# Performance work log

Hardware: AMD Instinct MI355X
Metric: run time of the kernel (lower is better)

The kernel has to match this reference:

```python
import jax, jax.numpy as jnp
import numpy as np

N = 50000      # nodes
E = 1_600_000  # edges (avg degree 32)
H = 32         # hidden_dim
ED = 16        # edge_dim
L = 4          # num EGNN layers
F_IN = 23      # prot_in_dim
LN_EPS = 1e-5


def setup_inputs() -> dict:
    key = jax.random.key(0)
    ks = jax.random.split(key, 24)
    s = 0.1  # param init scale
    inp = {
        "node_pos": jax.random.normal(ks[0], (N, 3), jnp.float32) * 10.0,
        "node_feat": jax.random.normal(ks[1], (N, F_IN), jnp.float32),
        "edge_attr": jax.random.normal(ks[2], (E, ED), jnp.float32),
        "proj_w": jax.random.normal(ks[3], (F_IN, H), jnp.float32) * s,
        "proj_b": jnp.zeros((H,), jnp.float32),
        # phi_e: Linear(2H+ED+1 -> H), SiLU, Linear(H -> H)   [stacked over L layers]
        "pe_w1": jax.random.normal(ks[4], (L, 2 * H + ED + 1, H), jnp.float32) * s,
        "pe_b1": jnp.zeros((L, H), jnp.float32),
        "pe_w2": jax.random.normal(ks[5], (L, H, H), jnp.float32) * s,
        "pe_b2": jnp.zeros((L, H), jnp.float32),
        # phi_h: Linear(2H -> H), SiLU, Linear(H -> H)
        "ph_w1": jax.random.normal(ks[6], (L, 2 * H, H), jnp.float32) * s,
        "ph_b1": jnp.zeros((L, H), jnp.float32),
        "ph_w2": jax.random.normal(ks[7], (L, H, H), jnp.float32) * s,
        "ph_b2": jnp.zeros((L, H), jnp.float32),
        # phi_x: Linear(H -> H), SiLU, Linear(H -> 1)
        "px_w1": jax.random.normal(ks[8], (L, H, H), jnp.float32) * s,
        "px_b1": jnp.zeros((L, H), jnp.float32),
        "px_w2": jax.random.normal(ks[9], (L, H, 1), jnp.float32) * s,
        "px_b2": jnp.zeros((L, 1), jnp.float32),
        # LayerNorm per layer
        "ln_g": jnp.ones((L, H), jnp.float32),
        "ln_b": jnp.zeros((L, H), jnp.float32),
        "edge_index": jax.random.randint(ks[10], (2, E), 0, N, dtype=jnp.int32),
    }
    return inp


def _mlp2(x, w1, b1, w2, b2):
    # Linear -> SiLU -> Linear (dropout=0 / eval mode)
    return jax.nn.silu(x @ w1 + b1) @ w2 + b2


def _layernorm(x, g, b):
    mu = jnp.mean(x, axis=-1, keepdims=True)
    var = jnp.mean(jnp.square(x - mu), axis=-1, keepdims=True)
    return (x - mu) * jax.lax.rsqrt(var + LN_EPS) * g + b


def reference(node_pos, node_feat, edge_attr, proj_w, proj_b,
              pe_w1, pe_b1, pe_w2, pe_b2,
              ph_w1, ph_b1, ph_w2, ph_b2,
              px_w1, px_b1, px_w2, px_b2,
              ln_g, ln_b, edge_index):
    src = edge_index[0]
    dst = edge_index[1]
    n = node_feat.shape[0]

    h = node_feat @ proj_w + proj_b  # (N,H)
    x = node_pos                     # (N,3)

    for l in range(L):
        h_i = h[src]                 # (E,H)
        h_j = h[dst]                 # (E,H)
        x_i = x[src]                 # (E,3)
        x_j = x[dst]                 # (E,3)
        diff = x_j - x_i             # (E,3)
        dist = jnp.sqrt(jnp.sum(diff * diff, axis=-1, keepdims=True) + 1e-09)  # (E,1)

        m_in = jnp.concatenate([h_i, h_j, edge_attr, dist], axis=-1)  # (E, 2H+ED+1)
        m_ij = _mlp2(m_in, pe_w1[l], pe_b1[l], pe_w2[l], pe_b2[l])    # (E,H)

        agg = jax.ops.segment_sum(m_ij, dst, num_segments=n)          # (N,H)
        dh = _mlp2(jnp.concatenate([h, agg], axis=-1),
                   ph_w1[l], ph_b1[l], ph_w2[l], ph_b2[l])            # (N,H)
        h = _layernorm(h + dh, ln_g[l], ln_b[l])

        # coordinate update: x_j += sum_i unit(x_j - x_i) * phi_x(m_ij)
        dir_norm = jnp.linalg.norm(diff, axis=-1, keepdims=True) + 1e-09
        gate = _mlp2(m_ij, px_w1[l], px_b1[l], px_w2[l], px_b2[l])    # (E,1)
        coord_msg = (diff / dir_norm) * gate                          # (E,3)
        dx = jax.ops.segment_sum(coord_msg, dst, num_segments=n)      # (N,3)
        x = x + dx

    return h, x
```

## Files before the change

kernel.cpp:

```cpp
#include <hip/hip_runtime.h>
#include <hip/hip_fp16.h>
#include <math.h>

#define NN 50000
#define NE 1600000
#define H  32
#define ED 16
#define FIN 23
#define NL 4
#define CPAD 16
#define LW 19

union F4 { float4 v; float f[4]; };

__device__ __forceinline__ float silu_f(float v) {
    float e = __expf(-v);
    return v * __builtin_amdgcn_rcpf(1.0f + e);
}

__device__ __forceinline__ void acc4(float hid[H], float4 hv4, const float* __restrict__ w) {
    F4 u; u.v = hv4;
    #pragma unroll
    for (int jj = 0; jj < 4; ++jj) {
        float v = u.f[jj];
        #pragma unroll
        for (int k = 0; k < H; ++k) hid[k] = fmaf(v, w[jj * H + k], hid[k]);
    }
}


__global__ __launch_bounds__(256) void k_prep(
    const float* __restrict__ pe_w2, const float* __restrict__ pe_b2,
    const float* __restrict__ px_w1, const float* __restrict__ px_b1,
    float* __restrict__ w2x, float* __restrict__ cvec)
{
    int l = blockIdx.x;
    const float* w2  = pe_w2 + (size_t)l * H * H;
    const float* xw1 = px_w1 + (size_t)l * H * H;
    int tid = threadIdx.x;
    #pragma unroll
    for (int q = 0; q < 4; ++q) {
        int idx = q * 256 + tid;
        int j = idx >> 5, k = idx & 31;
        float acc = 0.0f;
        #pragma unroll
        for (int t = 0; t < H; ++t) acc = fmaf(w2[j * H + t], xw1[t * H + k], acc);
        w2x[(size_t)l * H * H + idx] = acc;
    }
    if (tid < H) {
        const float* b2 = pe_b2 + l * H;
        float acc = px_b1[l * H + tid];
        #pragma unroll
        for (int t = 0; t < H; ++t) acc = fmaf(b2[t], xw1[t * H + tid], acc);
        cvec[l * H + tid] = acc;
    }
}


__global__ __launch_bounds__(256) void k_hist(
    const int* __restrict__ edst, int* __restrict__ cnt, int* __restrict__ rank)
{
    int e = blockIdx.x * 256 + threadIdx.x;
    if (e >= NE) return;
    rank[e] = atomicAdd(&cnt[(size_t)edst[e] * CPAD], 1);
}

__global__ __launch_bounds__(1024) void k_scan(
    const int* __restrict__ cnt, int* __restrict__ rs)
{
    __shared__ int wsum[16];
    __shared__ int s_carry;
    int t = threadIdx.x;
    int lane = t & 63, wid = t >> 6;
    if (t == 0) s_carry = 0;
    __syncthreads();
    for (int base = 0; base < NN; base += 1024) {
        int i = base + t;
        int v = (i < NN) ? cnt[(size_t)i * CPAD] : 0;
        int incl = v;
        #pragma unroll
        for (int off = 1; off < 64; off <<= 1) {
            int u = __shfl_up(incl, off, 64);
            if (lane >= off) incl += u;
        }
        if (lane == 63) wsum[wid] = incl;
        __syncthreads();
        int wpre = 0;
        #pragma unroll
        for (int w = 0; w < 16; ++w) { int ws = wsum[w]; wpre += (w < wid) ? ws : 0; }
        int carry = s_carry;
        if (i < NN) rs[i] = carry + wpre + incl - v;
        __syncthreads();
        if (t == 1023) s_carry = carry + wpre + incl;
        __syncthreads();
    }
    if (t == 0) rs[NN] = s_carry;
}

__global__ __launch_bounds__(256) void k_scatter2(
    const int* __restrict__ esrc, const int* __restrict__ edst,
    const int* __restrict__ rank, const int* __restrict__ rs,
    const float* __restrict__ ea,
    float* __restrict__ ea_s, unsigned int* __restrict__ sdp)
{
    int e = blockIdx.x * 256 + threadIdx.x;
    if (e >= NE) return;
    int s = esrc[e], d = edst[e];
    int slot = rs[d] + rank[e];
    const float4* src4 = (const float4*)(ea + (size_t)e * ED);
    float4* dst4 = (float4*)(ea_s + (size_t)slot * ED);
    #pragma unroll
    for (int j = 0; j < ED / 4; ++j) dst4[j] = src4[j];
    sdp[slot] = (unsigned int)s | ((unsigned int)d << 16);
}


__global__ __launch_bounds__(256) void proj2(
    const float* __restrict__ feat, const float* __restrict__ pos,
    const float* __restrict__ W, const float* __restrict__ bias,
    const float* __restrict__ pew1,
    float* __restrict__ h, float* __restrict__ a, float* __restrict__ b,
    float4* __restrict__ xp)
{
    int n = blockIdx.x * 256 + threadIdx.x;
    if (n >= NN) return;
    float acc[H];
    #pragma unroll
    for (int k = 0; k < H; ++k) acc[k] = bias[k];
    #pragma unroll 1
    for (int j = 0; j < FIN; ++j) {
        float v = feat[n * FIN + j];
        const float* w = W + j * H;
        #pragma unroll
        for (int k = 0; k < H; ++k) acc[k] = fmaf(v, w[k], acc[k]);
    }
    float4* h4 = (float4*)(h + (size_t)n * H);
    #pragma unroll
    for (int k4 = 0; k4 < H / 4; ++k4) {
        float4 o;
        o.x = acc[4*k4+0]; o.y = acc[4*k4+1]; o.z = acc[4*k4+2]; o.w = acc[4*k4+3];
        h4[k4] = o;
    }
    float pa[H];
    #pragma unroll
    for (int k = 0; k < H; ++k) pa[k] = 0.0f;
    #pragma unroll 1
    for (int j = 0; j < H; ++j) {
        float v = acc[j];
        const float* w = pew1 + j * H;
        #pragma unroll
        for (int k = 0; k < H; ++k) pa[k] = fmaf(v, w[k], pa[k]);
    }
    float4* a4 = (float4*)(a + (size_t)n * H);
    #pragma unroll
    for (int k4 = 0; k4 < H / 4; ++k4) {
        float4 o;
        o.x = pa[4*k4+0]; o.y = pa[4*k4+1]; o.z = pa[4*k4+2]; o.w = pa[4*k4+3];
        a4[k4] = o;
    }
    #pragma unroll
    for (int k = 0; k < H; ++k) pa[k] = 0.0f;
    #pragma unroll 1
    for (int j = 0; j < H; ++j) {
        float v = acc[j];
        const float* w = pew1 + (H + j) * H;
        #pragma unroll
        for (int k = 0; k < H; ++k) pa[k] = fmaf(v, w[k], pa[k]);
    }
    float4* b4 = (float4*)(b + (size_t)n * H);
    #pragma unroll
    for (int k4 = 0; k4 < H / 4; ++k4) {
        float4 o;
        o.x = pa[4*k4+0]; o.y = pa[4*k4+1]; o.z = pa[4*k4+2]; o.w = pa[4*k4+3];
        b4[k4] = o;
    }
    float4 xo;
    xo.x = pos[3*n+0]; xo.y = pos[3*n+1]; xo.z = pos[3*n+2]; xo.w = 0.0f;
    xp[n] = xo;
}


__global__ __launch_bounds__(256) void egnn_edge5(
    const float* __restrict__ a, const float* __restrict__ b,
    const float4* __restrict__ xp,
    const float* __restrict__ ea_s, const unsigned int* __restrict__ sdp,
    const float* __restrict__ w1, const float* __restrict__ b1,
    const float* __restrict__ w2x, const float* __restrict__ cvec,
    const float* __restrict__ xw2, const float* __restrict__ xb2,
    float* __restrict__ agg, float* __restrict__ dxb)
{
    __shared__ unsigned int ldsu[256 * LW];
    __shared__ int s_start[4][66];
    __shared__ int s_dstv[4][64];
    __shared__ int s_nseg[4];

    int tid = threadIdx.x;
    int w = tid >> 6, lane = tid & 63;
    int slot = blockIdx.x * 256 + tid;

    unsigned int sd = sdp[slot];
    int s = (int)(sd & 0xffffu), d = (int)(sd >> 16);

    float hid[H];
    const float4* av = (const float4*)(a + (size_t)s * H);
    const float4* bv = (const float4*)(b + (size_t)d * H);
    #pragma unroll
    for (int k4 = 0; k4 < H / 4; ++k4) {
        F4 ua, ub; ua.v = av[k4]; ub.v = bv[k4];
        #pragma unroll
        for (int jj = 0; jj < 4; ++jj)
            hid[4*k4+jj] = b1[4*k4+jj] + ua.f[jj] + ub.f[jj];
    }

    const float4* eav = (const float4*)(ea_s + (size_t)slot * ED);
    #pragma unroll 1
    for (int j4 = 0; j4 < ED / 4; ++j4)
        acc4(hid, eav[j4], w1 + (2 * H + j4 * 4) * H);

    float4 xi = xp[s];
    float4 xj = xp[d];
    float d0 = xj.x - xi.x, d1 = xj.y - xi.y, d2 = xj.z - xi.z;
    float sq = d0*d0 + d1*d1 + d2*d2;
    float dist = __builtin_amdgcn_sqrtf(sq + 1e-9f);
    {
        const float* wl = w1 + (2 * H + ED) * H;
        #pragma unroll
        for (int k = 0; k < H; ++k) hid[k] = fmaf(dist, wl[k], hid[k]);
    }

    float sarr[H];
    float gh[H];
    #pragma unroll
    for (int k = 0; k < H; ++k) gh[k] = cvec[k];
    #pragma unroll
    for (int j = 0; j < H; ++j) {
        float v = silu_f(hid[j]);
        sarr[j] = v;
        const float* ww = w2x + j * H;
        #pragma unroll
        for (int k = 0; k < H; ++k) gh[k] = fmaf(v, ww[k], gh[k]);
    }

    float gate = xb2[0];
    #pragma unroll
    for (int j = 0; j < H; ++j) gate = fmaf(silu_f(gh[j]), xw2[j], gate);
    float scale = gate * __builtin_amdgcn_rcpf(__builtin_amdgcn_sqrtf(sq) + 1e-9f);

    unsigned int* row = &ldsu[tid * LW];
    #pragma unroll
    for (int k2 = 0; k2 < 16; ++k2) {
        __half2 hh = __floats2half2_rn(sarr[2*k2], sarr[2*k2+1]);
        row[k2] = *reinterpret_cast<unsigned int*>(&hh);
    }
    row[16] = __float_as_uint(d0 * scale);
    row[17] = __float_as_uint(d1 * scale);
    row[18] = __float_as_uint(d2 * scale);

    int dprev = __shfl_up(d, 1, 64);
    bool flag = (lane == 0) || (d != dprev);
    unsigned long long ball = __ballot(flag);
    unsigned long long mask_le = (lane == 63) ? ~0ull : ((1ull << (lane + 1)) - 1ull);
    int segid = __popcll(ball & mask_le) - 1;
    if (flag) { s_start[w][segid] = lane; s_dstv[w][segid] = d; }
    if (lane == 0) {
        int ns = __popcll(ball);
        s_start[w][ns] = 64;
        s_nseg[w] = ns;
    }
    __syncthreads();

    int nseg = s_nseg[w];
    const unsigned int* wrows = &ldsu[(w * 64) * LW];
    int sub = lane >> 5, col = lane & 31;
    int word = col >> 1, sh = (col & 1) * 16;
    #pragma unroll 1
    for (int sg = sub; sg < nseg; sg += 2) {
        int r0 = s_start[w][sg], r1 = s_start[w][sg + 1];
        float v = 0.0f;
        #pragma unroll 1
        for (int r = r0; r < r1; ++r) {
            unsigned int u = wrows[r * LW + word];
            v += __half2float(__ushort_as_half((unsigned short)(u >> sh)));
        }
        unsafeAtomicAdd(&agg[(size_t)s_dstv[w][sg] * H + col], v);
    }
    #pragma unroll 1
    for (int j = lane; j < nseg * 4; j += 64) {
        int sg = j >> 2, c = j & 3;
        if (c < 3) {
            int r0 = s_start[w][sg], r1 = s_start[w][sg + 1];
            float v = 0.0f;
            #pragma unroll 1
            for (int r = r0; r < r1; ++r) v += __uint_as_float(wrows[r * LW + 16 + c]);
            unsafeAtomicAdd(&dxb[(size_t)s_dstv[w][sg] * 4 + c], v);
        }
    }
}


__global__ __launch_bounds__(256) void egnn_node5(
    const float* __restrict__ h, const float* __restrict__ agg,
    const float4* __restrict__ xin, const float* __restrict__ dxb,
    const int* __restrict__ rs,
    const float* __restrict__ ew2, const float* __restrict__ eb2,
    const float* __restrict__ w1, const float* __restrict__ b1,
    const float* __restrict__ w2, const float* __restrict__ b2,
    const float* __restrict__ lng, const float* __restrict__ lnb,
    const float* __restrict__ nxtw1, int last,
    float* __restrict__ hout, float* __restrict__ xout,
    float* __restrict__ aout, float* __restrict__ bout)
{
    int n = blockIdx.x * 256 + threadIdx.x;
    if (n >= NN) return;
    const float4* h4 = (const float4*)(h + (size_t)n * H);
    const float4* a4 = (const float4*)(agg + (size_t)n * H);

    float degf = (float)(rs[n + 1] - rs[n]);
    float ma[H];
    #pragma unroll
    for (int k = 0; k < H; ++k) ma[k] = degf * eb2[k];
    #pragma unroll 1
    for (int j4 = 0; j4 < H / 4; ++j4)
        acc4(ma, a4[j4], ew2 + (j4 * 4) * H);

    float hv[H];
    float hid[H];
    #pragma unroll
    for (int k = 0; k < H; ++k) hid[k] = b1[k];
    #pragma unroll 1
    for (int j4 = 0; j4 < H / 4; ++j4) {
        F4 u; u.v = h4[j4];
        #pragma unroll
        for (int jj = 0; jj < 4; ++jj) hv[4*j4+jj] = u.f[jj];
        acc4(hid, u.v, w1 + (j4 * 4) * H);
    }
    #pragma unroll
    for (int j = 0; j < H; ++j) {
        float v = ma[j];
        const float* ww = w1 + (H + j) * H;
        #pragma unroll
        for (int k = 0; k < H; ++k) hid[k] = fmaf(v, ww[k], hid[k]);
    }

    float dh[H];
    #pragma unroll
    for (int k = 0; k < H; ++k) dh[k] = b2[k];
    #pragma unroll
    for (int j = 0; j < H; ++j) {
        float v = silu_f(hid[j]);
        const float* ww = w2 + j * H;
        #pragma unroll
        for (int k = 0; k < H; ++k) dh[k] = fmaf(v, ww[k], dh[k]);
    }

    float y[H];
    float mu = 0.0f;
    #pragma unroll
    for (int k = 0; k < H; ++k) { y[k] = hv[k] + dh[k]; mu += y[k]; }
    mu *= (1.0f / H);
    float var = 0.0f;
    #pragma unroll
    for (int k = 0; k < H; ++k) { float t = y[k] - mu; var += t * t; }
    var *= (1.0f / H);
    float rstd = rsqrtf(var + 1e-5f);

    float hn[H];
    #pragma unroll
    for (int k = 0; k < H; ++k) hn[k] = (y[k] - mu) * rstd * lng[k] + lnb[k];

    float4* ho4 = (float4*)(hout + (size_t)n * H);
    #pragma unroll
    for (int k4 = 0; k4 < H / 4; ++k4) {
        float4 o;
        o.x = hn[4*k4+0]; o.y = hn[4*k4+1]; o.z = hn[4*k4+2]; o.w = hn[4*k4+3];
        ho4[k4] = o;
    }

    float4 xi = xin[n];
    float nx0 = xi.x + dxb[(size_t)n * 4 + 0];
    float nx1 = xi.y + dxb[(size_t)n * 4 + 1];
    float nx2 = xi.z + dxb[(size_t)n * 4 + 2];
    if (last) {
        xout[3*n+0] = nx0; xout[3*n+1] = nx1; xout[3*n+2] = nx2;
    } else {
        float4 o; o.x = nx0; o.y = nx1; o.z = nx2; o.w = 0.0f;
        ((float4*)xout)[n] = o;
    }

    if (!last) {
        float pa[H];
        #pragma unroll
        for (int k = 0; k < H; ++k) pa[k] = 0.0f;
        #pragma unroll 1
        for (int j = 0; j < H; ++j) {
            float v = hn[j];
            const float* ww = nxtw1 + j * H;
            #pragma unroll
            for (int k = 0; k < H; ++k) pa[k] = fmaf(v, ww[k], pa[k]);
        }
        float4* ao4 = (float4*)(aout + (size_t)n * H);
        #pragma unroll
        for (int k4 = 0; k4 < H / 4; ++k4) {
            float4 o;
            o.x = pa[4*k4+0]; o.y = pa[4*k4+1]; o.z = pa[4*k4+2]; o.w = pa[4*k4+3];
            ao4[k4] = o;
        }
        #pragma unroll
        for (int k = 0; k < H; ++k) pa[k] = 0.0f;
        #pragma unroll 1
        for (int j = 0; j < H; ++j) {
            float v = hn[j];
            const float* ww = nxtw1 + (H + j) * H;
            #pragma unroll
            for (int k = 0; k < H; ++k) pa[k] = fmaf(v, ww[k], pa[k]);
        }
        float4* bo4 = (float4*)(bout + (size_t)n * H);
        #pragma unroll
        for (int k4 = 0; k4 < H / 4; ++k4) {
            float4 o;
            o.x = pa[4*k4+0]; o.y = pa[4*k4+1]; o.z = pa[4*k4+2]; o.w = pa[4*k4+3];
            bo4[k4] = o;
        }
    }
}

extern "C" void kernel_launch(void* const* d_in, const int* in_sizes, int n_in,
                              void* d_out, int out_size, void* d_ws, size_t ws_size,
                              hipStream_t stream) {
    const float* node_pos  = (const float*)d_in[0];
    const float* node_feat = (const float*)d_in[1];
    const float* edge_attr = (const float*)d_in[2];
    const float* proj_w    = (const float*)d_in[3];
    const float* proj_b    = (const float*)d_in[4];
    const float* pe_w1     = (const float*)d_in[5];
    const float* pe_b1     = (const float*)d_in[6];
    const float* pe_w2     = (const float*)d_in[7];
    const float* pe_b2     = (const float*)d_in[8];
    const float* ph_w1     = (const float*)d_in[9];
    const float* ph_b1     = (const float*)d_in[10];
    const float* ph_w2     = (const float*)d_in[11];
    const float* ph_b2     = (const float*)d_in[12];
    const float* px_w1     = (const float*)d_in[13];
    const float* px_b1     = (const float*)d_in[14];
    const float* px_w2     = (const float*)d_in[15];
    const float* px_b2     = (const float*)d_in[16];
    const float* ln_g      = (const float*)d_in[17];
    const float* ln_b      = (const float*)d_in[18];
    const int*   eidx      = (const int*)d_in[19];
    const int*   esrc      = eidx;
    const int*   edst      = eidx + NE;

    float* out_h = (float*)d_out;
    float* out_x = out_h + (size_t)NN * H;

    size_t off = 0;
    float* ea_s = (float*)d_ws;                off += (size_t)NE * ED;
    unsigned int* sdp = (unsigned int*)((float*)d_ws + off); off += NE;
    float* abuf = (float*)d_ws + off;          off += (size_t)NN * H;
    float* bbuf = (float*)d_ws + off;          off += (size_t)NN * H;
    float* h_a  = (float*)d_ws + off;          off += (size_t)NN * H;
    float* h_b  = (float*)d_ws + off;          off += (size_t)NN * H;
    float4* xp_a = (float4*)((float*)d_ws + off); off += (size_t)NN * 4;
    float4* xp_b = (float4*)((float*)d_ws + off); off += (size_t)NN * 4;
    float* agg  = (float*)d_ws + off;          off += (size_t)NN * H;
    float* dxb  = (float*)d_ws + off;          off += (size_t)NN * 4;
    float* w2x  = (float*)d_ws + off;          off += (size_t)NL * H * H;
    float* cvec = (float*)d_ws + off;          off += (size_t)NL * H;
    int*   cnt  = (int*)((float*)d_ws + off);  off += (size_t)NN * CPAD;
    int*   rs   = (int*)((float*)d_ws + off);  off += NN + 4;
    int*   rank = (int*)((float*)d_ws + off);  off += NE;

    dim3 nblk((NN + 255) / 256), eblk(NE / 256);

    hipMemsetAsync(cnt, 0, (size_t)NN * CPAD * sizeof(int), stream);
    k_hist<<<eblk, 256, 0, stream>>>(edst, cnt, rank);
    k_scan<<<1, 1024, 0, stream>>>(cnt, rs);
    k_scatter2<<<eblk, 256, 0, stream>>>(esrc, edst, rank, rs, edge_attr, ea_s, sdp);
    k_prep<<<dim3(NL), 256, 0, stream>>>(pe_w2, pe_b2, px_w1, px_b1, w2x, cvec);

    proj2<<<nblk, 256, 0, stream>>>(node_feat, node_pos, proj_w, proj_b, pe_w1,
                                    h_a, abuf, bbuf, xp_a);

    const float* hcur = h_a;
    const float4* xcur = xp_a;
    float* hbufs[2] = { h_b, h_a };
    float4* xbufs[2] = { xp_b, xp_a };

    for (int l = 0; l < NL; ++l) {
        hipMemsetAsync(agg, 0, (size_t)NN * (H + 4) * sizeof(float), stream);
        egnn_edge5<<<eblk, 256, 0, stream>>>(abuf, bbuf, xcur, ea_s, sdp,
            pe_w1 + (size_t)l * (2*H + ED + 1) * H, pe_b1 + l * H,
            w2x + (size_t)l * H * H,               cvec + l * H,
            px_w2 + (size_t)l * H,                 px_b2 + l,
            agg, dxb);
        int last = (l == NL - 1);
        float* ho = last ? out_h : hbufs[l & 1];
        float* xo = last ? out_x : (float*)xbufs[l & 1];
        const float* nxtw1 = last ? pe_w1 : (pe_w1 + (size_t)(l + 1) * (2*H + ED + 1) * H);
        egnn_node5<<<nblk, 256, 0, stream>>>(hcur, agg, xcur, dxb, rs,
            pe_w2 + (size_t)l * H * H, pe_b2 + l * H,
            ph_w1 + (size_t)l * 2 * H * H, ph_b1 + l * H,
            ph_w2 + (size_t)l * H * H,     ph_b2 + l * H,
            ln_g + l * H, ln_b + l * H,
            nxtw1, last, ho, xo, abuf, bbuf);
        hcur = ho;
        xcur = xbufs[l & 1];
    }
}
```

Baseline: 1.160 ms.

## Use packed fp16 dot products for edge MLP and restructure segment reduction

Edge attributes and the fused w2·px_w1 weight are stored as packed fp16 pairs, so the edge kernel's inner products use v_dot2 instructions, halving FMA count and edge-attribute bandwidth. The segment reduction now walks the wave ballot mask directly with shuffles instead of building LDS segment tables behind a block barrier. The per-layer memset of agg/dxb is replaced by zeroing inside the node kernel after it reads them. This trades some accuracy, since more of the pipeline runs in fp16 with round-toward-zero packing, for less ALU work and fewer launches.

```diff
diff --git a/kernel.cpp b/kernel.cpp
--- a/kernel.cpp
+++ b/kernel.cpp
@@ -8,10 +8,24 @@
 #define ED 16
 #define FIN 23
 #define NL 4
+#define W1ROWS 81
 #define CPAD 16
 #define LW 19
 
+typedef _Float16 hv2 __attribute__((ext_vector_type(2)));
+typedef __fp16   fv2 __attribute__((ext_vector_type(2)));
+union H2U { unsigned int u; hv2 h; fv2 f; };
 union F4 { float4 v; float f[4]; };
+
+__device__ __forceinline__ unsigned int pack2(float a, float b) {
+    H2U r; r.f = __builtin_amdgcn_cvt_pkrtz(a, b);
+    return r.u;
+}
+
+__device__ __forceinline__ float fdot2f(unsigned int a, unsigned int b, float c) {
+    H2U ua, ub; ua.u = a; ub.u = b;
+    return __builtin_amdgcn_fdot2(ua.h, ub.h, c, false);
+}
 
 __device__ __forceinline__ float silu_f(float v) {
     float e = __expf(-v);
@@ -30,10 +44,13 @@
 
 
 __global__ __launch_bounds__(256) void k_prep(
-    const float* __restrict__ pe_w2, const float* __restrict__ pe_b2,
+    const float* __restrict__ pe_w1, const float* __restrict__ pe_w2,
+    const float* __restrict__ pe_b2,
     const float* __restrict__ px_w1, const float* __restrict__ px_b1,
-    float* __restrict__ w2x, float* __restrict__ cvec)
-{
+    unsigned int* __restrict__ w1h, unsigned int* __restrict__ w2xh,
+    float* __restrict__ cvec)
+{
+    __shared__ float w2x[H * H];
     int l = blockIdx.x;
     const float* w2  = pe_w2 + (size_t)l * H * H;
     const float* xw1 = px_w1 + (size_t)l * H * H;
@@ -45,11 +62,23 @@
         float acc = 0.0f;
         #pragma unroll
         for (int t = 0; t < H; ++t) acc = fmaf(w2[j * H + t], xw1[t * H + k], acc);
-        w2x[(size_t)l * H * H + idx] = acc;
+        w2x[idx] = acc;
+    }
+    __syncthreads();
+    #pragma unroll
+    for (int q = 0; q < 2; ++q) {
+        int i2 = q * 256 + tid;
+        int j2 = i2 >> 5, k = i2 & 31;
+        w2xh[(size_t)l * 512 + i2] = pack2(w2x[(2*j2) * H + k], w2x[(2*j2+1) * H + k]);
+    }
+    {
+        int j2 = tid >> 5, k = tid & 31;
+        const float* w1 = pe_w1 + (size_t)l * W1ROWS * H;
+        w1h[(size_t)l * 256 + tid] = pack2(w1[(2*H + 2*j2) * H + k], w1[(2*H + 2*j2+1) * H + k]);
     }
     if (tid < H) {
+        float acc = px_b1[l * H + tid];
         const float* b2 = pe_b2 + l * H;
-        float acc = px_b1[l * H + tid];
         #pragma unroll
         for (int t = 0; t < H; ++t) acc = fmaf(b2[t], xw1[t * H + tid], acc);
         cvec[l * H + tid] = acc;
@@ -101,16 +130,20 @@
     const int* __restrict__ esrc, const int* __restrict__ edst,
     const int* __restrict__ rank, const int* __restrict__ rs,
     const float* __restrict__ ea,
-    float* __restrict__ ea_s, unsigned int* __restrict__ sdp)
+    unsigned int* __restrict__ ea_h, unsigned int* __restrict__ sdp)
 {
     int e = blockIdx.x * 256 + threadIdx.x;
     if (e >= NE) return;
     int s = esrc[e], d = edst[e];
     int slot = rs[d] + rank[e];
     const float4* src4 = (const float4*)(ea + (size_t)e * ED);
-    float4* dst4 = (float4*)(ea_s + (size_t)slot * ED);
-    #pragma unroll
-    for (int j = 0; j < ED / 4; ++j) dst4[j] = src4[j];
+    uint2* dst2 = (uint2*)(ea_h + (size_t)slot * 8);
+    #pragma unroll
+    for (int j = 0; j < ED / 4; ++j) {
+        float4 v = src4[j];
+        uint2 o; o.x = pack2(v.x, v.y); o.y = pack2(v.z, v.w);
+        dst2[j] = o;
+    }
     sdp[slot] = (unsigned int)s | ((unsigned int)d << 16);
 }
 
@@ -180,19 +213,17 @@
 }
 
 
-__global__ __launch_bounds__(256) void egnn_edge5(
+__global__ __launch_bounds__(256) void egnn_edge6(
     const float* __restrict__ a, const float* __restrict__ b,
     const float4* __restrict__ xp,
-    const float* __restrict__ ea_s, const unsigned int* __restrict__ sdp,
-    const float* __restrict__ w1, const float* __restrict__ b1,
-    const float* __restrict__ w2x, const float* __restrict__ cvec,
+    const unsigned int* __restrict__ ea_h, const unsigned int* __restrict__ sdp,
+    const unsigned int* __restrict__ w1h, const float* __restrict__ b1,
+    const float* __restrict__ w1,
+    const unsigned int* __restrict__ w2xh, const float* __restrict__ cvec,
     const float* __restrict__ xw2, const float* __restrict__ xb2,
     float* __restrict__ agg, float* __restrict__ dxb)
 {
-    __shared__ unsigned int ldsu[256 * LW];
-    __shared__ int s_start[4][66];
-    __shared__ int s_dstv[4][64];
-    __shared__ int s_nseg[4];
+    __shared__ unsigned int ldsu[256 * LW + 4];
 
     int tid = threadIdx.x;
     int w = tid >> 6, lane = tid & 63;
@@ -212,10 +243,16 @@
             hid[4*k4+jj] = b1[4*k4+jj] + ua.f[jj] + ub.f[jj];
     }
 
-    const float4* eav = (const float4*)(ea_s + (size_t)slot * ED);
-    #pragma unroll 1
-    for (int j4 = 0; j4 < ED / 4; ++j4)
-        acc4(hid, eav[j4], w1 + (2 * H + j4 * 4) * H);
+    const uint4* ev = (const uint4*)(ea_h + (size_t)slot * 8);
+    uint4 e0 = ev[0], e1 = ev[1];
+    unsigned int ew[8] = { e0.x, e0.y, e0.z, e0.w, e1.x, e1.y, e1.z, e1.w };
+    #pragma unroll 1
+    for (int j2 = 0; j2 < 8; ++j2) {
+        unsigned int ea2 = ew[j2];
+        const unsigned int* wr = w1h + j2 * H;
+        #pragma unroll
+        for (int k = 0; k < H; ++k) hid[k] = fdot2f(ea2, wr[k], hid[k]);
+    }
 
     float4 xi = xp[s];
     float4 xj = xp[d];
@@ -228,17 +265,20 @@
         for (int k = 0; k < H; ++k) hid[k] = fmaf(dist, wl[k], hid[k]);
     }
 
-    float sarr[H];
+    unsigned int sp[16];
+    #pragma unroll
+    for (int j2 = 0; j2 < 16; ++j2)
+        sp[j2] = pack2(silu_f(hid[2*j2]), silu_f(hid[2*j2+1]));
+
     float gh[H];
     #pragma unroll
     for (int k = 0; k < H; ++k) gh[k] = cvec[k];
-    #pragma unroll
-    for (int j = 0; j < H; ++j) {
-        float v = silu_f(hid[j]);
-        sarr[j] = v;
-        const float* ww = w2x + j * H;
-        #pragma unroll
-        for (int k = 0; k < H; ++k) gh[k] = fmaf(v, ww[k], gh[k]);
+    #pragma unroll 1
+    for (int j2 = 0; j2 < 16; ++j2) {
+        unsigned int sv = sp[j2];
+        const unsigned int* wr = w2xh + j2 * H;
+        #pragma unroll
+        for (int k = 0; k < H; ++k) gh[k] = fdot2f(sv, wr[k], gh[k]);
     }
 
     float gate = xb2[0];
@@ -248,10 +288,7 @@
 
     unsigned int* row = &ldsu[tid * LW];
     #pragma unroll
-    for (int k2 = 0; k2 < 16; ++k2) {
-        __half2 hh = __floats2half2_rn(sarr[2*k2], sarr[2*k2+1]);
-        row[k2] = *reinterpret_cast<unsigned int*>(&hh);
-    }
+    for (int k2 = 0; k2 < 16; ++k2) row[k2] = sp[k2];
     row[16] = __float_as_uint(d0 * scale);
     row[17] = __float_as_uint(d1 * scale);
     row[18] = __float_as_uint(d2 * scale);
@@ -259,48 +296,46 @@
     int dprev = __shfl_up(d, 1, 64);
     bool flag = (lane == 0) || (d != dprev);
     unsigned long long ball = __ballot(flag);
-    unsigned long long mask_le = (lane == 63) ? ~0ull : ((1ull << (lane + 1)) - 1ull);
-    int segid = __popcll(ball & mask_le) - 1;
-    if (flag) { s_start[w][segid] = lane; s_dstv[w][segid] = d; }
-    if (lane == 0) {
-        int ns = __popcll(ball);
-        s_start[w][ns] = 64;
-        s_nseg[w] = ns;
-    }
-    __syncthreads();
-
-    int nseg = s_nseg[w];
+
+    int half = lane >> 5, col = lane & 31;
+    int word = col >> 1, sh = (col & 1) * 16;
+    int c = lane & 3, strip = lane >> 2;
     const unsigned int* wrows = &ldsu[(w * 64) * LW];
-    int sub = lane >> 5, col = lane & 31;
-    int word = col >> 1, sh = (col & 1) * 16;
-    #pragma unroll 1
-    for (int sg = sub; sg < nseg; sg += 2) {
-        int r0 = s_start[w][sg], r1 = s_start[w][sg + 1];
+
+    unsigned long long cur = ball;
+    while (cur) {
+        int r0 = (int)__builtin_ctzll(cur);
+        unsigned long long nxt = cur & (cur - 1);
+        int r1 = nxt ? (int)__builtin_ctzll(nxt) : 64;
+        int dseg = __shfl(d, r0, 64);
+
         float v = 0.0f;
         #pragma unroll 1
-        for (int r = r0; r < r1; ++r) {
+        for (int r = r0 + half; r < r1; r += 2) {
             unsigned int u = wrows[r * LW + word];
             v += __half2float(__ushort_as_half((unsigned short)(u >> sh)));
         }
-        unsafeAtomicAdd(&agg[(size_t)s_dstv[w][sg] * H + col], v);
-    }
-    #pragma unroll 1
-    for (int j = lane; j < nseg * 4; j += 64) {
-        int sg = j >> 2, c = j & 3;
-        if (c < 3) {
-            int r0 = s_start[w][sg], r1 = s_start[w][sg + 1];
-            float v = 0.0f;
-            #pragma unroll 1
-            for (int r = r0; r < r1; ++r) v += __uint_as_float(wrows[r * LW + 16 + c]);
-            unsafeAtomicAdd(&dxb[(size_t)s_dstv[w][sg] * 4 + c], v);
-        }
-    }
-}
-
-
-__global__ __launch_bounds__(256) void egnn_node5(
-    const float* __restrict__ h, const float* __restrict__ agg,
-    const float4* __restrict__ xin, const float* __restrict__ dxb,
+        v += __shfl_xor(v, 32, 64);
+        if (lane < 32) unsafeAtomicAdd(&agg[(size_t)dseg * H + col], v);
+
+        float cv = 0.0f;
+        #pragma unroll 1
+        for (int r = r0 + strip; r < r1; r += 16)
+            cv += __uint_as_float(wrows[r * LW + 16 + c]);
+        cv += __shfl_xor(cv, 4, 64);
+        cv += __shfl_xor(cv, 8, 64);
+        cv += __shfl_xor(cv, 16, 64);
+        cv += __shfl_xor(cv, 32, 64);
+        if (lane < 3) unsafeAtomicAdd(&dxb[(size_t)dseg * 4 + c], cv);
+
+        cur = nxt;
+    }
+}
+
+
+__global__ __launch_bounds__(256) void egnn_node6(
+    const float* __restrict__ h, float* __restrict__ agg,
+    const float4* __restrict__ xin, float* __restrict__ dxb,
     const int* __restrict__ rs,
     const float* __restrict__ ew2, const float* __restrict__ eb2,
     const float* __restrict__ w1, const float* __restrict__ b1,
@@ -313,7 +348,7 @@
     int n = blockIdx.x * 256 + threadIdx.x;
     if (n >= NN) return;
     const float4* h4 = (const float4*)(h + (size_t)n * H);
-    const float4* a4 = (const float4*)(agg + (size_t)n * H);
+    float4* a4 = (float4*)(agg + (size_t)n * H);
 
     float degf = (float)(rs[n + 1] - rs[n]);
     float ma[H];
@@ -322,6 +357,10 @@
     #pragma unroll 1
     for (int j4 = 0; j4 < H / 4; ++j4)
         acc4(ma, a4[j4], ew2 + (j4 * 4) * H);
+
+    float4 z; z.x = 0.0f; z.y = 0.0f; z.z = 0.0f; z.w = 0.0f;
+    #pragma unroll
+    for (int j4 = 0; j4 < H / 4; ++j4) a4[j4] = z;
 
     float hv[H];
     float hid[H];
@@ -380,6 +419,7 @@
     float nx0 = xi.x + dxb[(size_t)n * 4 + 0];
     float nx1 = xi.y + dxb[(size_t)n * 4 + 1];
     float nx2 = xi.z + dxb[(size_t)n * 4 + 2];
+    ((float4*)dxb)[n] = z;
     if (last) {
         xout[3*n+0] = nx0; xout[3*n+1] = nx1; xout[3*n+2] = nx2;
     } else {
@@ -454,7 +494,7 @@
     float* out_x = out_h + (size_t)NN * H;
 
     size_t off = 0;
-    float* ea_s = (float*)d_ws;                off += (size_t)NE * ED;
+    unsigned int* ea_h = (unsigned int*)d_ws;   off += (size_t)NE * 8;
     unsigned int* sdp = (unsigned int*)((float*)d_ws + off); off += NE;
     float* abuf = (float*)d_ws + off;          off += (size_t)NN * H;
     float* bbuf = (float*)d_ws + off;          off += (size_t)NN * H;
@@ -464,7 +504,8 @@
     float4* xp_b = (float4*)((float*)d_ws + off); off += (size_t)NN * 4;
     float* agg  = (float*)d_ws + off;          off += (size_t)NN * H;
     float* dxb  = (float*)d_ws + off;          off += (size_t)NN * 4;
-    float* w2x  = (float*)d_ws + off;          off += (size_t)NL * H * H;
+    unsigned int* w1h  = (unsigned int*)((float*)d_ws + off); off += (size_t)NL * 256;
+    unsigned int* w2xh = (unsigned int*)((float*)d_ws + off); off += (size_t)NL * 512;
     float* cvec = (float*)d_ws + off;          off += (size_t)NL * H;
     int*   cnt  = (int*)((float*)d_ws + off);  off += (size_t)NN * CPAD;
     int*   rs   = (int*)((float*)d_ws + off);  off += NN + 4;
@@ -473,10 +514,11 @@
     dim3 nblk((NN + 255) / 256), eblk(NE / 256);
 
     hipMemsetAsync(cnt, 0, (size_t)NN * CPAD * sizeof(int), stream);
+    hipMemsetAsync(agg, 0, (size_t)NN * (H + 4) * sizeof(float), stream);
     k_hist<<<eblk, 256, 0, stream>>>(edst, cnt, rank);
     k_scan<<<1, 1024, 0, stream>>>(cnt, rs);
-    k_scatter2<<<eblk, 256, 0, stream>>>(esrc, edst, rank, rs, edge_attr, ea_s, sdp);
-    k_prep<<<dim3(NL), 256, 0, stream>>>(pe_w2, pe_b2, px_w1, px_b1, w2x, cvec);
+    k_scatter2<<<eblk, 256, 0, stream>>>(esrc, edst, rank, rs, edge_attr, ea_h, sdp);
+    k_prep<<<dim3(NL), 256, 0, stream>>>(pe_w1, pe_w2, pe_b2, px_w1, px_b1, w1h, w2xh, cvec);
 
     proj2<<<nblk, 256, 0, stream>>>(node_feat, node_pos, proj_w, proj_b, pe_w1,
                                     h_a, abuf, bbuf, xp_a);
@@ -487,17 +529,17 @@
     float4* xbufs[2] = { xp_b, xp_a };
 
     for (int l = 0; l < NL; ++l) {
-        hipMemsetAsync(agg, 0, (size_t)NN * (H + 4) * sizeof(float), stream);
-        egnn_edge5<<<eblk, 256, 0, stream>>>(abuf, bbuf, xcur, ea_s, sdp,
-            pe_w1 + (size_t)l * (2*H + ED + 1) * H, pe_b1 + l * H,
-            w2x + (size_t)l * H * H,               cvec + l * H,
-            px_w2 + (size_t)l * H,                 px_b2 + l,
+        egnn_edge6<<<eblk, 256, 0, stream>>>(abuf, bbuf, xcur, ea_h, sdp,
+            w1h + (size_t)l * 256, pe_b1 + l * H,
+            pe_w1 + (size_t)l * W1ROWS * H,
+            w2xh + (size_t)l * 512, cvec + l * H,
+            px_w2 + (size_t)l * H,  px_b2 + l,
             agg, dxb);
         int last = (l == NL - 1);
         float* ho = last ? out_h : hbufs[l & 1];
         float* xo = last ? out_x : (float*)xbufs[l & 1];
-        const float* nxtw1 = last ? pe_w1 : (pe_w1 + (size_t)(l + 1) * (2*H + ED + 1) * H);
-        egnn_node5<<<nblk, 256, 0, stream>>>(hcur, agg, xcur, dxb, rs,
+        const float* nxtw1 = last ? pe_w1 : (pe_w1 + (size_t)(l + 1) * W1ROWS * H);
+        egnn_node6<<<nblk, 256, 0, stream>>>(hcur, agg, xcur, dxb, rs,
             pe_w2 + (size_t)l * H * H, pe_b2 + l * H,
             ph_w1 + (size_t)l * 2 * H * H, ph_b1 + l * H,
             ph_w2 + (size_t)l * H * H,     ph_b2 + l * H,
```

After: 1.005 ms. 1.15x faster.
